# Optimization experiments

Hardware: AMD Instinct MI355X
Metric: run time of the kernel (lower is better)

The kernel has to match this reference:

```python
import jax, jax.numpy as jnp
import numpy as np

BETA = 0.9          # snn.Leaky default-ish decay given in module
THRESH = 1.0        # snntorch default threshold


def spike(x):
    # heaviside(x); surrogate grad handled in bwd module
    return (x > 0).astype(x.dtype)


def setup_inputs() -> dict:
    key = jax.random.key(0)
    ks = jax.random.split(key, 5)
    T, B, NI, NH, NO = 100, 512, 784, 1024, 10
    x = jax.random.normal(ks[0], (T, B, NI), dtype=jnp.float32)
    W1 = jax.random.normal(ks[1], (NH, NI), dtype=jnp.float32) / np.sqrt(NI)
    b1 = jax.random.normal(ks[2], (NH,), dtype=jnp.float32) * 0.01
    W2 = jax.random.normal(ks[3], (NO, NH), dtype=jnp.float32) / np.sqrt(NH)
    b2 = jax.random.normal(ks[4], (NO,), dtype=jnp.float32) * 0.01
    return {"x": x, "W1": W1, "b1": b1, "W2": W2, "b2": b2}


def reference(x, W1, b1, W2, b2):
    # x: [T, B, num_inputs]
    B = x.shape[1]
    NH = W1.shape[0]
    NO = W2.shape[0]
    dt = x.dtype

    def step(carry, xt):
        mem1, mem2 = carry
        cur1 = xt @ W1.T + b1                       # [B, NH]
        reset1 = (mem1 > THRESH).astype(dt)         # from previous mem
        mem1 = BETA * mem1 + cur1 - reset1 * THRESH
        spk1 = spike(mem1 - THRESH)
        cur2 = spk1 @ W2.T + b2                     # [B, NO]
        reset2 = (mem2 > THRESH).astype(dt)
        mem2 = BETA * mem2 + cur2 - reset2 * THRESH
        spk2 = spike(mem2 - THRESH)
        return (mem1, mem2), spk2

    init = (jnp.zeros((B, NH), dt), jnp.zeros((B, NO), dt))
    (_, mem2), spk2_rec = jax.lax.scan(step, init, x)
    return spk2_rec, mem2
```

## Files before the change

kernel.cpp:

```cpp
#include <hip/hip_runtime.h>
#include <hip/hip_bf16.h>

#define NI 784
#define NH 1024
#define NO 10
#define BATCH 512
#define TSTEPS 100

#define BM 128
#define BN 128
#define BK 16
#define LDT 132

typedef __attribute__((ext_vector_type(4))) float floatx4;
typedef __attribute__((ext_vector_type(2))) float floatx2;

static __device__ __forceinline__ floatx2 fma2(floatx2 a, floatx2 b, floatx2 c) {
#if __has_builtin(__builtin_elementwise_fma)
  return __builtin_elementwise_fma(a, b, c);
#else
  floatx2 r; r.x = fmaf(a.x, b.x, c.x); r.y = fmaf(a.y, b.y, c.y); return r;
#endif
}

__global__ __launch_bounds__(256) void init_ws_kernel(float* __restrict__ p, int n) {
  int i = blockIdx.x * 256 + threadIdx.x;
  if (i < n) p[i] = 0.0f;
}

__global__ __launch_bounds__(256) void sgemm1_kernel(
    const float* __restrict__ X,
    const float* __restrict__ W1,
    const float* __restrict__ b1,
    float* __restrict__ C)
{
  __shared__ __align__(16) float As[BK * LDT];
  __shared__ __align__(16) float Bs[BK * LDT];

  const int tid = threadIdx.x;
  const int tx = tid & 15;
  const int ty = tid >> 4;
  const int m0 = blockIdx.y * BM;
  const int n0 = blockIdx.x * BN;

  const int srow  = tid >> 2;
  const int skcol = (tid & 3) * 4;

  floatx2 acc[8][4];
#pragma unroll
  for (int i = 0; i < 8; ++i)
#pragma unroll
    for (int j = 0; j < 4; ++j) acc[i][j] = (floatx2){0.f, 0.f};

  for (int k0 = 0; k0 < NI; k0 += BK) {
    const floatx4 a0 = *(const floatx4*)&X [(size_t)(m0 + srow)      * NI + k0 + skcol];
    const floatx4 a1 = *(const floatx4*)&X [(size_t)(m0 + 64 + srow) * NI + k0 + skcol];
    const floatx4 w0 = *(const floatx4*)&W1[(size_t)(n0 + srow)      * NI + k0 + skcol];
    const floatx4 w1 = *(const floatx4*)&W1[(size_t)(n0 + 64 + srow) * NI + k0 + skcol];
    __syncthreads();
#pragma unroll
    for (int e = 0; e < 4; ++e) {
      As[(skcol + e) * LDT + srow]      = a0[e];
      As[(skcol + e) * LDT + 64 + srow] = a1[e];
      Bs[(skcol + e) * LDT + srow]      = w0[e];
      Bs[(skcol + e) * LDT + 64 + srow] = w1[e];
    }
    __syncthreads();

#pragma unroll
    for (int k = 0; k < BK; ++k) {
      const floatx4 av0 = *(const floatx4*)&As[k * LDT + ty * 8];
      const floatx4 av1 = *(const floatx4*)&As[k * LDT + ty * 8 + 4];
      const floatx4 bv0 = *(const floatx4*)&Bs[k * LDT + tx * 8];
      const floatx4 bv1 = *(const floatx4*)&Bs[k * LDT + tx * 8 + 4];
      const float a[8] = {av0[0], av0[1], av0[2], av0[3], av1[0], av1[1], av1[2], av1[3]};
      const floatx2 b2[4] = {{bv0[0], bv0[1]}, {bv0[2], bv0[3]},
                             {bv1[0], bv1[1]}, {bv1[2], bv1[3]}};
#pragma unroll
      for (int i = 0; i < 8; ++i) {
        const floatx2 ai = {a[i], a[i]};
#pragma unroll
        for (int j = 0; j < 4; ++j)
          acc[i][j] = fma2(ai, b2[j], acc[i][j]);
      }
    }
  }

#pragma unroll
  for (int i = 0; i < 8; ++i) {
    float* crow = &C[(size_t)(m0 + ty * 8 + i) * NH + n0 + tx * 8];
#pragma unroll
    for (int jj = 0; jj < 2; ++jj) {
      floatx4 v;
#pragma unroll
      for (int e = 0; e < 4; ++e)
        v[e] = acc[i][jj * 2 + (e >> 1)][0 ] , v[e] = 0.0f;
      v[0] = acc[i][jj * 2 + 0].x + b1[n0 + tx * 8 + jj * 4 + 0];
      v[1] = acc[i][jj * 2 + 0].y + b1[n0 + tx * 8 + jj * 4 + 1];
      v[2] = acc[i][jj * 2 + 1].x + b1[n0 + tx * 8 + jj * 4 + 2];
      v[3] = acc[i][jj * 2 + 1].y + b1[n0 + tx * 8 + jj * 4 + 3];
      *(floatx4*)&crow[jj * 4] = v;
    }
  }
}

__global__ __launch_bounds__(256) void recur_kernel(
    const float* __restrict__ cur1,
    const float* __restrict__ W2,
    const float* __restrict__ b2,
    float* __restrict__ mem1s,
    float* __restrict__ mem2s,
    float* __restrict__ out,
    long long out_size, int t0, int tc, int last)
{
  const int b    = blockIdx.x;
  const int tid  = threadIdx.x;
  const int lane = tid & 63;
  const int wave = tid >> 6;

  __shared__ float red[4][NO];

  float w[4][NO];
#pragma unroll
  for (int j = 0; j < 4; ++j)
#pragma unroll
    for (int o = 0; o < NO; ++o)
      w[j][o] = W2[o * NH + tid * 4 + j];

  floatx4 m1 = *(const floatx4*)&mem1s[(size_t)b * NH + tid * 4];
  float m2 = 0.0f, bb = 0.0f;
  if (tid < NO) {
    m2 = mem2s[b * NO + tid];
    bb = b2[tid];
  }

  const floatx4* c4 = (const floatx4*)cur1;

  for (int t = 0; t < tc; ++t) {
    const floatx4 c = c4[((size_t)t * BATCH + b) * (NH / 4) + tid];

    float a[NO];
#pragma unroll
    for (int o = 0; o < NO; ++o) a[o] = 0.0f;

#pragma unroll
    for (int j = 0; j < 4; ++j) {
      float mj = m1[j];
      float reset = (mj > 1.0f) ? 1.0f : 0.0f;
      mj = 0.9f * mj + c[j] - reset;
      m1[j] = mj;
      float s = (mj > 1.0f) ? 1.0f : 0.0f;
#pragma unroll
      for (int o = 0; o < NO; ++o) a[o] = fmaf(s, w[j][o], a[o]);
    }

#pragma unroll
    for (int m = 1; m <= 32; m <<= 1)
#pragma unroll
      for (int o = 0; o < NO; ++o) a[o] += __shfl_xor(a[o], m, 64);

    if (lane == 0) {
#pragma unroll
      for (int o = 0; o < NO; ++o) red[wave][o] = a[o];
    }
    __syncthreads();

    if (tid < NO) {
      float cur2 = red[0][tid] + red[1][tid] + red[2][tid] + red[3][tid] + bb;
      float reset2 = (m2 > 1.0f) ? 1.0f : 0.0f;
      m2 = 0.9f * m2 + cur2 - reset2;
      float spk2 = (m2 > 1.0f) ? 1.0f : 0.0f;
      long long idx = ((long long)(t0 + t) * BATCH + b) * NO + tid;
      if (idx < out_size) out[idx] = spk2;
    }
    __syncthreads();
  }

  *(floatx4*)&mem1s[(size_t)b * NH + tid * 4] = m1;
  if (tid < NO) {
    mem2s[b * NO + tid] = m2;
    if (last) {
      long long idx = (long long)TSTEPS * BATCH * NO + b * NO + tid;
      if (idx < out_size) out[idx] = m2;
    }
  }
}

__global__ __launch_bounds__(256) void fused_fp32_kernel(
    const float* __restrict__ x,
    const float* __restrict__ W1,
    const float* __restrict__ b1,
    const float* __restrict__ W2,
    const float* __restrict__ b2,
    float* __restrict__ out, long long out_size)
{
  const int b    = blockIdx.x;
  const int tid  = threadIdx.x;
  const int lane = tid & 63;
  const int wave = tid >> 6;

  __shared__ __align__(16) float xs[NI + 4];
  __shared__ float red[4][NO];

  float w[4][NO];
#pragma unroll
  for (int j = 0; j < 4; ++j)
#pragma unroll
    for (int o = 0; o < NO; ++o)
      w[j][o] = W2[o * NH + tid * 4 + j];

  float bias1[4];
#pragma unroll
  for (int j = 0; j < 4; ++j) bias1[j] = b1[tid * 4 + j];

  float m1[4] = {0.f, 0.f, 0.f, 0.f};
  float m2 = 0.0f, bb = 0.0f;
  if (tid < NO) bb = b2[tid];

  for (int t = 0; t < TSTEPS; ++t) {
    if (tid < 196)
      *(floatx4*)&xs[tid * 4] = *(const floatx4*)&x[((size_t)t * BATCH + b) * NI + tid * 4];
    __syncthreads();

    float a[NO];
#pragma unroll
    for (int o = 0; o < NO; ++o) a[o] = 0.0f;

#pragma unroll
    for (int j = 0; j < 4; ++j) {
      const float* wr = W1 + (size_t)(tid * 4 + j) * NI;
      float dot = 0.0f;
      for (int cch = 0; cch < 196; ++cch) {
        floatx4 wv = *(const floatx4*)&wr[cch * 4];
        floatx4 xv = *(const floatx4*)&xs[cch * 4];
#pragma unroll
        for (int e = 0; e < 4; ++e) dot = fmaf(wv[e], xv[e], dot);
      }
      float cur = dot + bias1[j];
      float mj = m1[j];
      float reset = (mj > 1.0f) ? 1.0f : 0.0f;
      mj = 0.9f * mj + cur - reset;
      m1[j] = mj;
      float s = (mj > 1.0f) ? 1.0f : 0.0f;
#pragma unroll
      for (int o = 0; o < NO; ++o) a[o] = fmaf(s, w[j][o], a[o]);
    }

#pragma unroll
    for (int m = 1; m <= 32; m <<= 1)
#pragma unroll
      for (int o = 0; o < NO; ++o) a[o] += __shfl_xor(a[o], m, 64);

    if (lane == 0) {
#pragma unroll
      for (int o = 0; o < NO; ++o) red[wave][o] = a[o];
    }
    __syncthreads();

    if (tid < NO) {
      float cur2 = red[0][tid] + red[1][tid] + red[2][tid] + red[3][tid] + bb;
      float reset2 = (m2 > 1.0f) ? 1.0f : 0.0f;
      m2 = 0.9f * m2 + cur2 - reset2;
      float spk2 = (m2 > 1.0f) ? 1.0f : 0.0f;
      long long idx = ((long long)t * BATCH + b) * NO + tid;
      if (idx < out_size) out[idx] = spk2;
    }
    __syncthreads();
  }

  if (tid < NO) {
    long long idx = (long long)TSTEPS * BATCH * NO + b * NO + tid;
    if (idx < out_size) out[idx] = m2;
  }
}

extern "C" void kernel_launch(void* const* d_in, const int* in_sizes, int n_in,
                              void* d_out, int out_size, void* d_ws, size_t ws_size,
                              hipStream_t stream) {
  const float* x  = (const float*)d_in[0];
  const float* W1 = (const float*)d_in[1];
  const float* b1 = (const float*)d_in[2];
  const float* W2 = (const float*)d_in[3];
  const float* b2 = (const float*)d_in[4];
  float* out = (float*)d_out;

  const size_t mem1_bytes = (size_t)BATCH * NH * 4;
  const size_t mem2_bytes = (size_t)BATCH * NO * 4;
  size_t fixed = (mem1_bytes + mem2_bytes + 255) & ~(size_t)255;
  const size_t per_step = (size_t)BATCH * NH * 4;

  if (d_ws == nullptr || ws_size < fixed + per_step) {
    fused_fp32_kernel<<<BATCH, 256, 0, stream>>>(x, W1, b1, W2, b2, out,
                                                 (long long)out_size);
    return;
  }

  char* ws = (char*)d_ws;
  float* mem1s = (float*)ws;
  float* mem2s = (float*)(ws + mem1_bytes);
  float* cur1  = (float*)(ws + fixed);

  int Tc = (int)((ws_size - fixed) / per_step);
  if (Tc > TSTEPS) Tc = TSTEPS;

  const int nInit = BATCH * NH + BATCH * NO;
  init_ws_kernel<<<(nInit + 255) / 256, 256, 0, stream>>>((float*)ws, nInit);

  for (int t0 = 0; t0 < TSTEPS; t0 += Tc) {
    const int tc = (TSTEPS - t0 < Tc) ? (TSTEPS - t0) : Tc;
    const int M = tc * BATCH;
    dim3 g(NH / BN, M / BM);
    sgemm1_kernel<<<g, 256, 0, stream>>>(x + (size_t)t0 * BATCH * NI, W1, b1, cur1);
    recur_kernel<<<BATCH, 256, 0, stream>>>(cur1, W2, b2, mem1s, mem2s, out,
                                            (long long)out_size, t0, tc,
                                            (t0 + tc >= TSTEPS) ? 1 : 0);
  }
}
```

Measured before the change: 1.341 ms.

## Enlarge SGEMM tile to 128x256 with register prefetch; prefetch cur1 in recurrence

The input-projection SGEMM moves from 128x128 to 128x256 block tiles, giving each thread a 16x8 scalar-FMA micro-tile instead of the packed 8x4 floatx2 one. It also loads the next K-slice of X and W1 into registers while the current shared-memory tile is being computed. The recurrent kernel now prefetches the next timestep's cur1 vector before processing the current one, to hide global load latency. The larger tile raises register pressure, halves the number of column blocks, and drops the packed FMA path.

```diff
diff --git a/kernel.cpp b/kernel.cpp
--- a/kernel.cpp
+++ b/kernel.cpp
@@ -8,100 +8,111 @@
 #define TSTEPS 100
 
 #define BM 128
-#define BN 128
+#define BN 256
 #define BK 16
-#define LDT 132
+#define LDA 132
+#define LDB 260
 
 typedef __attribute__((ext_vector_type(4))) float floatx4;
-typedef __attribute__((ext_vector_type(2))) float floatx2;
-
-static __device__ __forceinline__ floatx2 fma2(floatx2 a, floatx2 b, floatx2 c) {
-#if __has_builtin(__builtin_elementwise_fma)
-  return __builtin_elementwise_fma(a, b, c);
-#else
-  floatx2 r; r.x = fmaf(a.x, b.x, c.x); r.y = fmaf(a.y, b.y, c.y); return r;
-#endif
-}
 
 __global__ __launch_bounds__(256) void init_ws_kernel(float* __restrict__ p, int n) {
   int i = blockIdx.x * 256 + threadIdx.x;
   if (i < n) p[i] = 0.0f;
 }
 
-__global__ __launch_bounds__(256) void sgemm1_kernel(
+__global__ __launch_bounds__(256, 2) void sgemm1_kernel(
     const float* __restrict__ X,
     const float* __restrict__ W1,
     const float* __restrict__ b1,
     float* __restrict__ C)
 {
-  __shared__ __align__(16) float As[BK * LDT];
-  __shared__ __align__(16) float Bs[BK * LDT];
+  __shared__ __align__(16) float As[BK * LDA];
+  __shared__ __align__(16) float Bs[BK * LDB];
 
   const int tid = threadIdx.x;
-  const int tx = tid & 15;
-  const int ty = tid >> 4;
+  const int tx = tid & 31;
+  const int ty = tid >> 5;
+  const int n0 = blockIdx.x * BN;
   const int m0 = blockIdx.y * BM;
-  const int n0 = blockIdx.x * BN;
 
   const int srow  = tid >> 2;
   const int skcol = (tid & 3) * 4;
 
-  floatx2 acc[8][4];
-#pragma unroll
-  for (int i = 0; i < 8; ++i)
-#pragma unroll
-    for (int j = 0; j < 4; ++j) acc[i][j] = (floatx2){0.f, 0.f};
-
-  for (int k0 = 0; k0 < NI; k0 += BK) {
-    const floatx4 a0 = *(const floatx4*)&X [(size_t)(m0 + srow)      * NI + k0 + skcol];
-    const floatx4 a1 = *(const floatx4*)&X [(size_t)(m0 + 64 + srow) * NI + k0 + skcol];
-    const floatx4 w0 = *(const floatx4*)&W1[(size_t)(n0 + srow)      * NI + k0 + skcol];
-    const floatx4 w1 = *(const floatx4*)&W1[(size_t)(n0 + 64 + srow) * NI + k0 + skcol];
+  float acc[16][8];
+#pragma unroll
+  for (int i = 0; i < 16; ++i)
+#pragma unroll
+    for (int j = 0; j < 8; ++j) acc[i][j] = 0.0f;
+
+  const float* Xs  = X  + (size_t)m0 * NI + skcol;
+  const float* W1s = W1 + (size_t)n0 * NI + skcol;
+
+  floatx4 xa0 = *(const floatx4*)&Xs [(size_t)(srow)      * NI];
+  floatx4 xa1 = *(const floatx4*)&Xs [(size_t)(64 + srow) * NI];
+  floatx4 wq0 = *(const floatx4*)&W1s[(size_t)(srow)       * NI];
+  floatx4 wq1 = *(const floatx4*)&W1s[(size_t)(64 + srow)  * NI];
+  floatx4 wq2 = *(const floatx4*)&W1s[(size_t)(128 + srow) * NI];
+  floatx4 wq3 = *(const floatx4*)&W1s[(size_t)(192 + srow) * NI];
+
+  for (int kt = 0; kt < NI / BK; ++kt) {
     __syncthreads();
 #pragma unroll
     for (int e = 0; e < 4; ++e) {
-      As[(skcol + e) * LDT + srow]      = a0[e];
-      As[(skcol + e) * LDT + 64 + srow] = a1[e];
-      Bs[(skcol + e) * LDT + srow]      = w0[e];
-      Bs[(skcol + e) * LDT + 64 + srow] = w1[e];
-    }
-    __syncthreads();
+      As[(skcol + e) * LDA + srow]       = xa0[e];
+      As[(skcol + e) * LDA + 64 + srow]  = xa1[e];
+      Bs[(skcol + e) * LDB + srow]       = wq0[e];
+      Bs[(skcol + e) * LDB + 64 + srow]  = wq1[e];
+      Bs[(skcol + e) * LDB + 128 + srow] = wq2[e];
+      Bs[(skcol + e) * LDB + 192 + srow] = wq3[e];
+    }
+    __syncthreads();
+
+    if (kt + 1 < NI / BK) {
+      const int k0 = (kt + 1) * BK;
+      xa0 = *(const floatx4*)&Xs [(size_t)(srow)      * NI + k0];
+      xa1 = *(const floatx4*)&Xs [(size_t)(64 + srow) * NI + k0];
+      wq0 = *(const floatx4*)&W1s[(size_t)(srow)       * NI + k0];
+      wq1 = *(const floatx4*)&W1s[(size_t)(64 + srow)  * NI + k0];
+      wq2 = *(const floatx4*)&W1s[(size_t)(128 + srow) * NI + k0];
+      wq3 = *(const floatx4*)&W1s[(size_t)(192 + srow) * NI + k0];
+    }
 
 #pragma unroll
     for (int k = 0; k < BK; ++k) {
-      const floatx4 av0 = *(const floatx4*)&As[k * LDT + ty * 8];
-      const floatx4 av1 = *(const floatx4*)&As[k * LDT + ty * 8 + 4];
-      const floatx4 bv0 = *(const floatx4*)&Bs[k * LDT + tx * 8];
-      const floatx4 bv1 = *(const floatx4*)&Bs[k * LDT + tx * 8 + 4];
-      const float a[8] = {av0[0], av0[1], av0[2], av0[3], av1[0], av1[1], av1[2], av1[3]};
-      const floatx2 b2[4] = {{bv0[0], bv0[1]}, {bv0[2], bv0[3]},
-                             {bv1[0], bv1[1]}, {bv1[2], bv1[3]}};
-#pragma unroll
-      for (int i = 0; i < 8; ++i) {
-        const floatx2 ai = {a[i], a[i]};
-#pragma unroll
-        for (int j = 0; j < 4; ++j)
-          acc[i][j] = fma2(ai, b2[j], acc[i][j]);
+      floatx4 av[4], bv[2];
+#pragma unroll
+      for (int h = 0; h < 4; ++h)
+        av[h] = *(const floatx4*)&As[k * LDA + 32 * h + ty * 4];
+#pragma unroll
+      for (int g = 0; g < 2; ++g)
+        bv[g] = *(const floatx4*)&Bs[k * LDB + 128 * g + tx * 4];
+#pragma unroll
+      for (int h = 0; h < 4; ++h)
+#pragma unroll
+        for (int i = 0; i < 4; ++i)
+#pragma unroll
+          for (int g = 0; g < 2; ++g)
+#pragma unroll
+            for (int j = 0; j < 4; ++j)
+              acc[h * 4 + i][g * 4 + j] =
+                  fmaf(av[h][i], bv[g][j], acc[h * 4 + i][g * 4 + j]);
+    }
+  }
+
+#pragma unroll
+  for (int h = 0; h < 4; ++h)
+#pragma unroll
+    for (int i = 0; i < 4; ++i) {
+      const int m = m0 + 32 * h + ty * 4 + i;
+#pragma unroll
+      for (int g = 0; g < 2; ++g) {
+        const int n = n0 + 128 * g + tx * 4;
+        floatx4 v;
+#pragma unroll
+        for (int j = 0; j < 4; ++j) v[j] = acc[h * 4 + i][g * 4 + j] + b1[n + j];
+        *(floatx4*)&C[(size_t)m * NH + n] = v;
       }
     }
-  }
-
-#pragma unroll
-  for (int i = 0; i < 8; ++i) {
-    float* crow = &C[(size_t)(m0 + ty * 8 + i) * NH + n0 + tx * 8];
-#pragma unroll
-    for (int jj = 0; jj < 2; ++jj) {
-      floatx4 v;
-#pragma unroll
-      for (int e = 0; e < 4; ++e)
-        v[e] = acc[i][jj * 2 + (e >> 1)][0 ] , v[e] = 0.0f;
-      v[0] = acc[i][jj * 2 + 0].x + b1[n0 + tx * 8 + jj * 4 + 0];
-      v[1] = acc[i][jj * 2 + 0].y + b1[n0 + tx * 8 + jj * 4 + 1];
-      v[2] = acc[i][jj * 2 + 1].x + b1[n0 + tx * 8 + jj * 4 + 2];
-      v[3] = acc[i][jj * 2 + 1].y + b1[n0 + tx * 8 + jj * 4 + 3];
-      *(floatx4*)&crow[jj * 4] = v;
-    }
-  }
 }
 
 __global__ __launch_bounds__(256) void recur_kernel(
@@ -135,9 +146,11 @@
   }
 
   const floatx4* c4 = (const floatx4*)cur1;
+  floatx4 c = c4[((size_t)0 * BATCH + b) * (NH / 4) + tid];
 
   for (int t = 0; t < tc; ++t) {
-    const floatx4 c = c4[((size_t)t * BATCH + b) * (NH / 4) + tid];
+    floatx4 cn = {0.f, 0.f, 0.f, 0.f};
+    if (t + 1 < tc) cn = c4[((size_t)(t + 1) * BATCH + b) * (NH / 4) + tid];
 
     float a[NO];
 #pragma unroll
@@ -174,6 +187,7 @@
       if (idx < out_size) out[idx] = spk2;
     }
     __syncthreads();
+    c = cn;
   }
 
   *(floatx4*)&mem1s[(size_t)b * NH + tid * 4] = m1;
```

After: 2.745 ms. 2.05x slower.

## Prefetch next tiles in SGEMM and recurrence, split B fragment for bank conflicts

Applied to the files above, without the earlier changes.

The SGEMM now loads the next K-tile from global memory into registers while computing on the current shared-memory tile, which hides global load latency. Each thread's B columns are split into two groups of 4, at tx*4 and 64+tx*4, instead of 8 contiguous columns, to reduce LDS bank conflicts. The packed float2 FMAs are replaced with scalar fmaf. The recurrence kernel also prefetches the next timestep's cur1 before computing the current step. This adds register pressure and may lose the packed-FMA throughput.

```diff
diff --git a/kernel.cpp b/kernel.cpp
--- a/kernel.cpp
+++ b/kernel.cpp
@@ -13,15 +13,6 @@
 #define LDT 132
 
 typedef __attribute__((ext_vector_type(4))) float floatx4;
-typedef __attribute__((ext_vector_type(2))) float floatx2;
-
-static __device__ __forceinline__ floatx2 fma2(floatx2 a, floatx2 b, floatx2 c) {
-#if __has_builtin(__builtin_elementwise_fma)
-  return __builtin_elementwise_fma(a, b, c);
-#else
-  floatx2 r; r.x = fmaf(a.x, b.x, c.x); r.y = fmaf(a.y, b.y, c.y); return r;
-#endif
-}
 
 __global__ __launch_bounds__(256) void init_ws_kernel(float* __restrict__ p, int n) {
   int i = blockIdx.x * 256 + threadIdx.x;
@@ -40,67 +31,74 @@
   const int tid = threadIdx.x;
   const int tx = tid & 15;
   const int ty = tid >> 4;
+  const int n0 = blockIdx.x * BN;
   const int m0 = blockIdx.y * BM;
-  const int n0 = blockIdx.x * BN;
 
   const int srow  = tid >> 2;
   const int skcol = (tid & 3) * 4;
 
-  floatx2 acc[8][4];
+  float acc[8][8];
 #pragma unroll
   for (int i = 0; i < 8; ++i)
 #pragma unroll
-    for (int j = 0; j < 4; ++j) acc[i][j] = (floatx2){0.f, 0.f};
-
-  for (int k0 = 0; k0 < NI; k0 += BK) {
-    const floatx4 a0 = *(const floatx4*)&X [(size_t)(m0 + srow)      * NI + k0 + skcol];
-    const floatx4 a1 = *(const floatx4*)&X [(size_t)(m0 + 64 + srow) * NI + k0 + skcol];
-    const floatx4 w0 = *(const floatx4*)&W1[(size_t)(n0 + srow)      * NI + k0 + skcol];
-    const floatx4 w1 = *(const floatx4*)&W1[(size_t)(n0 + 64 + srow) * NI + k0 + skcol];
+    for (int j = 0; j < 8; ++j) acc[i][j] = 0.0f;
+
+  const float* Xs  = X  + (size_t)m0 * NI + skcol;
+  const float* W1s = W1 + (size_t)n0 * NI + skcol;
+
+  floatx4 xa0 = *(const floatx4*)&Xs [(size_t)(srow)      * NI];
+  floatx4 xa1 = *(const floatx4*)&Xs [(size_t)(64 + srow) * NI];
+  floatx4 wq0 = *(const floatx4*)&W1s[(size_t)(srow)      * NI];
+  floatx4 wq1 = *(const floatx4*)&W1s[(size_t)(64 + srow) * NI];
+
+  for (int kt = 0; kt < NI / BK; ++kt) {
     __syncthreads();
 #pragma unroll
     for (int e = 0; e < 4; ++e) {
-      As[(skcol + e) * LDT + srow]      = a0[e];
-      As[(skcol + e) * LDT + 64 + srow] = a1[e];
-      Bs[(skcol + e) * LDT + srow]      = w0[e];
-      Bs[(skcol + e) * LDT + 64 + srow] = w1[e];
-    }
-    __syncthreads();
+      As[(skcol + e) * LDT + srow]      = xa0[e];
+      As[(skcol + e) * LDT + 64 + srow] = xa1[e];
+      Bs[(skcol + e) * LDT + srow]      = wq0[e];
+      Bs[(skcol + e) * LDT + 64 + srow] = wq1[e];
+    }
+    __syncthreads();
+
+    if (kt + 1 < NI / BK) {
+      const int k0 = (kt + 1) * BK;
+      xa0 = *(const floatx4*)&Xs [(size_t)(srow)      * NI + k0];
+      xa1 = *(const floatx4*)&Xs [(size_t)(64 + srow) * NI + k0];
+      wq0 = *(const floatx4*)&W1s[(size_t)(srow)      * NI + k0];
+      wq1 = *(const floatx4*)&W1s[(size_t)(64 + srow) * NI + k0];
+    }
 
 #pragma unroll
     for (int k = 0; k < BK; ++k) {
       const floatx4 av0 = *(const floatx4*)&As[k * LDT + ty * 8];
       const floatx4 av1 = *(const floatx4*)&As[k * LDT + ty * 8 + 4];
-      const floatx4 bv0 = *(const floatx4*)&Bs[k * LDT + tx * 8];
-      const floatx4 bv1 = *(const floatx4*)&Bs[k * LDT + tx * 8 + 4];
-      const float a[8] = {av0[0], av0[1], av0[2], av0[3], av1[0], av1[1], av1[2], av1[3]};
-      const floatx2 b2[4] = {{bv0[0], bv0[1]}, {bv0[2], bv0[3]},
-                             {bv1[0], bv1[1]}, {bv1[2], bv1[3]}};
-#pragma unroll
-      for (int i = 0; i < 8; ++i) {
-        const floatx2 ai = {a[i], a[i]};
-#pragma unroll
-        for (int j = 0; j < 4; ++j)
-          acc[i][j] = fma2(ai, b2[j], acc[i][j]);
-      }
+      const floatx4 bv0 = *(const floatx4*)&Bs[k * LDT + tx * 4];
+      const floatx4 bv1 = *(const floatx4*)&Bs[k * LDT + 64 + tx * 4];
+      const float a[8] = {av0[0], av0[1], av0[2], av0[3],
+                          av1[0], av1[1], av1[2], av1[3]};
+#pragma unroll
+      for (int i = 0; i < 8; ++i)
+#pragma unroll
+        for (int j = 0; j < 4; ++j) {
+          acc[i][j]     = fmaf(a[i], bv0[j], acc[i][j]);
+          acc[i][4 + j] = fmaf(a[i], bv1[j], acc[i][4 + j]);
+        }
     }
   }
 
 #pragma unroll
   for (int i = 0; i < 8; ++i) {
-    float* crow = &C[(size_t)(m0 + ty * 8 + i) * NH + n0 + tx * 8];
-#pragma unroll
-    for (int jj = 0; jj < 2; ++jj) {
-      floatx4 v;
-#pragma unroll
-      for (int e = 0; e < 4; ++e)
-        v[e] = acc[i][jj * 2 + (e >> 1)][0 ] , v[e] = 0.0f;
-      v[0] = acc[i][jj * 2 + 0].x + b1[n0 + tx * 8 + jj * 4 + 0];
-      v[1] = acc[i][jj * 2 + 0].y + b1[n0 + tx * 8 + jj * 4 + 1];
-      v[2] = acc[i][jj * 2 + 1].x + b1[n0 + tx * 8 + jj * 4 + 2];
-      v[3] = acc[i][jj * 2 + 1].y + b1[n0 + tx * 8 + jj * 4 + 3];
-      *(floatx4*)&crow[jj * 4] = v;
-    }
+    const int m = m0 + ty * 8 + i;
+    floatx4 v0, v1;
+#pragma unroll
+    for (int j = 0; j < 4; ++j) {
+      v0[j] = acc[i][j]     + b1[n0 + tx * 4 + j];
+      v1[j] = acc[i][4 + j] + b1[n0 + 64 + tx * 4 + j];
+    }
+    *(floatx4*)&C[(size_t)m * NH + n0 + tx * 4]      = v0;
+    *(floatx4*)&C[(size_t)m * NH + n0 + 64 + tx * 4] = v1;
   }
 }
 
@@ -135,9 +133,11 @@
   }
 
   const floatx4* c4 = (const floatx4*)cur1;
+  floatx4 c = c4[((size_t)0 * BATCH + b) * (NH / 4) + tid];
 
   for (int t = 0; t < tc; ++t) {
-    const floatx4 c = c4[((size_t)t * BATCH + b) * (NH / 4) + tid];
+    floatx4 cn = {0.f, 0.f, 0.f, 0.f};
+    if (t + 1 < tc) cn = c4[((size_t)(t + 1) * BATCH + b) * (NH / 4) + tid];
 
     float a[NO];
 #pragma unroll
@@ -174,6 +174,7 @@
       if (idx < out_size) out[idx] = spk2;
     }
     __syncthreads();
+    c = cn;
   }
 
   *(floatx4*)&mem1s[(size_t)b * NH + tid * 4] = m1;
```

After: 1.283 ms. 4.4% less time.
